# Kernel tuning notes

Measured on AMD Instinct MI355X. Metric: run time of the kernel, lower is better.

## Reference

```python
import jax, jax.numpy as jnp
import numpy as np

B, C, T = 4, 512, 4096
N2 = 32          # d_state // 2 complex modes
H = 2048         # hidden_channels
EPS = 1e-5


def setup_inputs() -> dict:
    key = jax.random.key(0)
    ks = jax.random.split(key, 8)
    dt_min, dt_max = 1e-3, 1e-1
    log_dt = jax.random.uniform(ks[1], (C,)) * (np.log(dt_max) - np.log(dt_min)) + np.log(dt_min)
    return {
        "x": jax.random.normal(ks[0], (B, C, T), jnp.float32),
        # ChannelwiseLayerNorm affine params
        "gamma": jnp.ones((C,), jnp.float32),
        "beta": jnp.zeros((C,), jnp.float32),
        # S4D kernel params (standard S4D-Lin init)
        "log_dt": log_dt.astype(jnp.float32),
        "C_re": jax.random.normal(ks[2], (C, N2), jnp.float32),
        "C_im": jax.random.normal(ks[3], (C, N2), jnp.float32),
        "log_A_real": jnp.log(0.5 * jnp.ones((C, N2), jnp.float32)),
        "A_imag": jnp.tile(jnp.pi * jnp.arange(N2, dtype=jnp.float32), (C, 1)),
        "D": jax.random.normal(ks[4], (C,), jnp.float32),
        # S4D output linear (Conv1d k=1 -> 2C, then GLU over channels)
        "Wo": jax.random.normal(ks[5], (2 * C, C), jnp.float32) / np.sqrt(C),
        "bo": jnp.zeros((2 * C,), jnp.float32),
        # FC MLP: Linear(C->H), PReLU(H), Linear(H->C)
        "W1": jax.random.normal(ks[6], (H, C), jnp.float32) / np.sqrt(C),
        "b1": jnp.zeros((H,), jnp.float32),
        "prelu_a": 0.25 * jnp.ones((H,), jnp.float32),
        "W2": jax.random.normal(ks[7], (C, H), jnp.float32) / np.sqrt(H),
        "b2": jnp.zeros((C,), jnp.float32),
    }


def reference(x, gamma, beta, log_dt, C_re, C_im, log_A_real, A_imag, D,
              Wo, bo, W1, b1, prelu_a, W2, b2):
    # ---- ChannelwiseLayerNorm over the channel dim of [B, C, T] ----
    mean = jnp.mean(x, axis=1, keepdims=True)
    var = jnp.var(x, axis=1, keepdims=True)
    u = gamma[None, :, None] * (x - mean) * jax.lax.rsqrt(var + EPS) + beta[None, :, None]

    # ---- S4D: diagonal SSM kernel via Vandermonde, applied by FFT conv ----
    L = x.shape[-1]
    dt = jnp.exp(log_dt)[:, None]                       # [C, 1]
    A = -jnp.exp(log_A_real) + 1j * A_imag              # [C, N2] complex diag
    dtA = A * dt                                        # [C, N2]
    Cd = (C_re + 1j * C_im) * (jnp.exp(dtA) - 1.0) / A  # discretized C (ZOH)
    vand = jnp.exp(dtA[..., None] * jnp.arange(L, dtype=jnp.float32))  # [C, N2, L]
    K = 2.0 * jnp.einsum('hn,hnl->hl', Cd, vand).real   # [C, L]

    k_f = jnp.fft.rfft(K, n=2 * L)                      # [C, L+1]
    u_f = jnp.fft.rfft(u, n=2 * L)                      # [B, C, L+1]
    y = jnp.fft.irfft(u_f * k_f, n=2 * L)[..., :L]      # causal conv
    y = y + u * D[None, :, None]                        # skip connection
    y = jax.nn.gelu(y, approximate=False)
    # output linear (1x1 conv to 2C) + GLU over channel dim
    z = jnp.einsum('oc,bct->bot', Wo, y) + bo[None, :, None]
    y = z[:, :C] * jax.nn.sigmoid(z[:, C:])             # [B, C, T]

    # ---- FC MLP with PReLU (per hidden channel) ----
    y = y.transpose(0, 2, 1)                            # [B, T, C]
    h = y @ W1.T + b1                                   # [B, T, H]
    h = jnp.where(h >= 0, h, prelu_a * h)
    y = h @ W2.T + b2                                   # [B, T, C]

    return x + y.transpose(0, 2, 1)                     # residual, [B, C, T]
```

## Files before the change

### kernel.cpp

```cpp
#include <hip/hip_runtime.h>
#include <math.h>

#define BB 4
#define CC 512
#define TT 4096
#define NN2 32
#define HH 2048

typedef __bf16 bf8v __attribute__((ext_vector_type(8)));
typedef __bf16 bf4v __attribute__((ext_vector_type(4)));
typedef float  f4v  __attribute__((ext_vector_type(4)));
typedef unsigned short u16x8 __attribute__((ext_vector_type(8)));

__device__ __forceinline__ void gload16(const void* g, void* l){
  __builtin_amdgcn_global_load_lds(
      (const __attribute__((address_space(1))) unsigned int*)g,
      (__attribute__((address_space(3))) unsigned int*)l, 16, 0, 0);
}
__device__ __forceinline__ float fast_gelu(float v){
  float x2 = v*v;
  float x  = 0.7978845608f*v*fmaf(0.044715f, x2, 1.0f);
  float t  = __expf(2.0f*x);
  return v - v*__builtin_amdgcn_rcpf(1.0f + t);
}
__device__ __forceinline__ float fast_sigmoid(float g){
  return __builtin_amdgcn_rcpf(1.0f + __expf(-g));
}
__device__ __forceinline__ unsigned short bfbits(float v){
  __bf16 h = (__bf16)v;
  return __builtin_bit_cast(unsigned short, h);
}

__global__ __launch_bounds__(256) void ln_kernel(
    const float* __restrict__ x, const float* __restrict__ gamma,
    const float* __restrict__ beta, __bf16* __restrict__ u)
{
  int tile = blockIdx.x & 63;
  int b    = blockIdx.x >> 6;
  int tl = threadIdx.x & 15;
  int cg = threadIdx.x >> 4;
  const float4* xp = (const float4*)(x + (size_t)b*CC*TT + tile*64) + tl;
  float4 s = {0,0,0,0}, s2 = {0,0,0,0};
  #pragma unroll 4
  for (int c = cg*32; c < (cg+1)*32; ++c){
    float4 v = xp[(size_t)c*(TT/4)];
    s.x += v.x; s.y += v.y; s.z += v.z; s.w += v.w;
    s2.x = fmaf(v.x,v.x,s2.x); s2.y = fmaf(v.y,v.y,s2.y);
    s2.z = fmaf(v.z,v.z,s2.z); s2.w = fmaf(v.w,v.w,s2.w);
  }
  __shared__ float4 ls[16][16], ls2[16][16], mean_s[16], inv_s[16];
  ls[cg][tl] = s; ls2[cg][tl] = s2;
  __syncthreads();
  if (threadIdx.x < 16){
    float4 ss = {0,0,0,0}, ss2 = {0,0,0,0};
    #pragma unroll
    for (int g2 = 0; g2 < 16; ++g2){
      float4 a = ls[g2][threadIdx.x], b2 = ls2[g2][threadIdx.x];
      ss.x+=a.x; ss.y+=a.y; ss.z+=a.z; ss.w+=a.w;
      ss2.x+=b2.x; ss2.y+=b2.y; ss2.z+=b2.z; ss2.w+=b2.w;
    }
    float4 mn, iv;
    mn.x = ss.x*(1.f/CC); mn.y = ss.y*(1.f/CC); mn.z = ss.z*(1.f/CC); mn.w = ss.w*(1.f/CC);
    iv.x = rsqrtf(ss2.x*(1.f/CC) - mn.x*mn.x + 1e-5f);
    iv.y = rsqrtf(ss2.y*(1.f/CC) - mn.y*mn.y + 1e-5f);
    iv.z = rsqrtf(ss2.z*(1.f/CC) - mn.z*mn.z + 1e-5f);
    iv.w = rsqrtf(ss2.w*(1.f/CC) - mn.w*mn.w + 1e-5f);
    mean_s[threadIdx.x] = mn; inv_s[threadIdx.x] = iv;
  }
  __syncthreads();
  float4 mn = mean_s[tl], iv = inv_s[tl];
  __bf16* up = u + (size_t)b*CC*TT + tile*64 + tl*4;
  #pragma unroll 4
  for (int c = cg*32; c < (cg+1)*32; ++c){
    float4 v = xp[(size_t)c*(TT/4)];
    float gi = gamma[c], be = beta[c];
    bf4v o;
    o[0] = (__bf16)fmaf(gi*iv.x, v.x - mn.x, be);
    o[1] = (__bf16)fmaf(gi*iv.y, v.y - mn.y, be);
    o[2] = (__bf16)fmaf(gi*iv.z, v.z - mn.z, be);
    o[3] = (__bf16)fmaf(gi*iv.w, v.w - mn.w, be);
    *(bf4v*)&up[(size_t)c*TT] = o;
  }
}

__global__ __launch_bounds__(256) void build_mats(
    const float* __restrict__ log_dt, const float* __restrict__ C_re,
    const float* __restrict__ C_im, const float* __restrict__ log_A_real,
    const float* __restrict__ A_imag, const float* __restrict__ Dp,
    __bf16* __restrict__ Tt, __bf16* __restrict__ V, __bf16* __restrict__ B2)
{
  __shared__ float cpart[4][64][33];
  __shared__ float kk[4][65];
  const int wv = threadIdx.x >> 6, lane = threadIdx.x & 63;
  const int c = blockIdx.x*4 + wv;
  const int m = lane & 31;
  float dt = expf(log_dt[c]);
  float Ar = -expf(log_A_real[c*NN2+m]);
  float Ai = A_imag[c*NN2+m];
  float er = expf(Ar*dt);
  float sw_, cw_; sincosf(Ai*dt, &sw_, &cw_);
  float wre = er*cw_, wim = er*sw_;
  float nr = wre-1.f, ni = wim;
  float inv = 1.f/(Ar*Ar + Ai*Ai);
  float qr = (nr*Ar + ni*Ai)*inv;
  float qi = (ni*Ar - nr*Ai)*inv;
  float Cr = C_re[c*NN2+m], Ci = C_im[c*NN2+m];
  float okr =  2.f*(Cr*qr - Ci*qi);
  float oki = -2.f*(Cr*qi + Ci*qr);
  __bf16* Ttc = Tt + (size_t)c*4096;
  __bf16* Vc  = V  + (size_t)c*4096;
  __bf16* B2c = B2 + (size_t)c*4096;
  if (lane < 32){
    float pre = 1.f, pim = 0.f;
    for (int l = 0; l <= 64; ++l){
      if (l <= 63){
        Vc[(2*m)*64   + (63-l)] = (__bf16)pre;
        Vc[(2*m+1)*64 + (63-l)] = (__bf16)pim;
      }
      float cR = fmaf(okr, pre,  oki*pim);
      float cQ = fmaf(oki, pre, -okr*pim);
      if (l <= 63) cpart[wv][l][m] = cR;
      if (l >= 1){
        B2c[(l-1)*64 + 2*m]   = (__bf16)cR;
        B2c[(l-1)*64 + 2*m+1] = (__bf16)cQ;
      }
      float npre = wre*pre - wim*pim;
      float npim = wre*pim + wim*pre;
      pre = npre; pim = npim;
    }
  }
  __syncthreads();
  float s = 0.f;
  #pragma unroll
  for (int mm = 0; mm < 32; ++mm) s += cpart[wv][lane][mm];
  if (lane == 0) s += Dp[c];
  kk[wv][lane] = s;
  __syncthreads();
  const int n = lane;
  #pragma unroll
  for (int kb = 0; kb < 8; ++kb){
    u16x8 v;
    #pragma unroll
    for (int e = 0; e < 8; ++e){
      int k = kb*8 + e;
      v[e] = bfbits((n >= k) ? kk[wv][n-k] : 0.f);
    }
    *(u16x8*)&Ttc[n*64 + kb*8] = v;
  }
}

__global__ __launch_bounds__(128) void s4dm_kernel(
    const __bf16* __restrict__ u, const float* __restrict__ log_dt,
    const float* __restrict__ log_A_real, const float* __restrict__ A_imag,
    const __bf16* __restrict__ Tt, const __bf16* __restrict__ V,
    const __bf16* __restrict__ B2, __bf16* __restrict__ gout)
{
  __shared__ __align__(16) float gbuf[2][64][66];
  __shared__ __align__(16) unsigned short s0buf[2][64][72];
  const int wv = threadIdx.x >> 6, l = threadIdx.x & 63;
  const int lr = l & 15, q = l >> 4;
  const int seq = blockIdx.x*2 + wv;
  const int c = seq & (CC-1);
  const __bf16* Up  = u  + (size_t)seq*TT;
  const __bf16* Ttc = Tt + (size_t)c*4096;
  const __bf16* Vc  = V  + (size_t)c*4096;
  const __bf16* B2c = B2 + (size_t)c*4096;

  f4v acc[4][4];
  #pragma unroll
  for (int a=0;a<4;++a)
    #pragma unroll
    for (int b=0;b<4;++b)
      #pragma unroll
      for (int r=0;r<4;++r) acc[a][b][r] = 0.f;

  #pragma unroll
  for (int kw = 0; kw < 2; ++kw){
    bf8v af[4], bv[4];
    #pragma unroll
    for (int mt=0;mt<4;++mt)
      af[mt] = *(const bf8v*)(Up + (mt*16+lr)*64 + kw*32 + q*8);
    #pragma unroll
    for (int nt=0;nt<4;++nt)
      bv[nt] = *(const bf8v*)(Vc + (nt*16+lr)*64 + kw*32 + q*8);
    #pragma unroll
    for (int mt=0;mt<4;++mt)
      #pragma unroll
      for (int nt=0;nt<4;++nt)
        acc[mt][nt] = __builtin_amdgcn_mfma_f32_16x16x32_bf16(af[mt], bv[nt], acc[mt][nt], 0,0,0);
  }
  #pragma unroll
  for (int mt=0;mt<4;++mt)
    #pragma unroll
    for (int nt=0;nt<4;++nt)
      #pragma unroll
      for (int r=0;r<4;++r)
        gbuf[wv][mt*16 + q*4 + r][nt*16 + lr] = acc[mt][nt][r];
  __syncthreads();

  if (l < 32){
    const int m = l;
    float dt = expf(log_dt[c]);
    float Ar = -expf(log_A_real[c*NN2+m]);
    float Ai = A_imag[c*NN2+m];
    float er = expf(Ar*dt);
    float sw_, cw_; sincosf(Ai*dt, &sw_, &cw_);
    float wr_ = er*cw_, wi_ = er*sw_;
    #pragma unroll
    for (int sq2=0;sq2<6;++sq2){
      float a=wr_, b=wi_;
      wr_ = a*a - b*b; wi_ = 2.f*a*b;
    }
    float S0r=0.f, S0i=0.f;
    for (int j=0;j<64;++j){
      float gr = gbuf[wv][j][2*m], gi = gbuf[wv][j][2*m+1];
      s0buf[wv][j][2*m]   = bfbits(S0r);
      s0buf[wv][j][2*m+1] = bfbits(S0i);
      float nRe = fmaf(wr_, S0r, fmaf(-wi_, S0i, gr));
      float nIm = fmaf(wr_, S0i, fmaf( wi_, S0r, gi));
      S0r = nRe; S0i = nIm;
    }
  }
  __syncthreads();

  #pragma unroll
  for (int a=0;a<4;++a)
    #pragma unroll
    for (int b=0;b<4;++b)
      #pragma unroll
      for (int r=0;r<4;++r) acc[a][b][r] = 0.f;
  #pragma unroll
  for (int kw = 0; kw < 2; ++kw){
    bf8v af[4], bv[4];
    #pragma unroll
    for (int mt=0;mt<4;++mt)
      af[mt] = *(const bf8v*)(Up + (mt*16+lr)*64 + kw*32 + q*8);
    #pragma unroll
    for (int nt=0;nt<4;++nt)
      bv[nt] = *(const bf8v*)(Ttc + (nt*16+lr)*64 + kw*32 + q*8);
    #pragma unroll
    for (int mt=0;mt<4;++mt)
      #pragma unroll
      for (int nt=0;nt<4;++nt)
        acc[mt][nt] = __builtin_amdgcn_mfma_f32_16x16x32_bf16(af[mt], bv[nt], acc[mt][nt], 0,0,0);
  }
  #pragma unroll
  for (int kw = 0; kw < 2; ++kw){
    bf8v af[4], bv[4];
    #pragma unroll
    for (int mt=0;mt<4;++mt)
      af[mt] = *(const bf8v*)&s0buf[wv][mt*16+lr][kw*32 + q*8];
    #pragma unroll
    for (int nt=0;nt<4;++nt)
      bv[nt] = *(const bf8v*)(B2c + (nt*16+lr)*64 + kw*32 + q*8);
    #pragma unroll
    for (int mt=0;mt<4;++mt)
      #pragma unroll
      for (int nt=0;nt<4;++nt)
        acc[mt][nt] = __builtin_amdgcn_mfma_f32_16x16x32_bf16(af[mt], bv[nt], acc[mt][nt], 0,0,0);
  }
  __syncthreads();

  unsigned short (*ybuf)[72] = (unsigned short(*)[72])&gbuf[wv][0][0];
  #pragma unroll
  for (int mt=0;mt<4;++mt)
    #pragma unroll
    for (int nt=0;nt<4;++nt)
      #pragma unroll
      for (int r=0;r<4;++r)
        ybuf[mt*16 + q*4 + r][nt*16 + lr] = bfbits(fast_gelu(acc[mt][nt][r]));
  __syncthreads();
  u16x8* dst = (u16x8*)(gout + (size_t)seq*TT);
  for (int i = l; i < 512; i += 64){
    int row = i >> 3, cq = i & 7;
    dst[i] = *(const u16x8*)&ybuf[row][cq*8];
  }
}

__global__ __launch_bounds__(256) void tr_kernel(const __bf16* __restrict__ gin,
                                                 __bf16* __restrict__ gout)
{
  __shared__ __align__(16) unsigned short ts[64][72];
  int bt = blockIdx.x;
  int bc = blockIdx.y;
  int b  = blockIdx.z;
  int tid = threadIdx.x;
  const __bf16* gp = gin + ((size_t)b*CC + bc*64)*TT + (size_t)bt*64;
  for (int i = tid; i < 512; i += 256){
    int c = i >> 3, tq = i & 7;
    u16x8 v = *(const u16x8*)(gp + (size_t)c*TT + tq*8);
    #pragma unroll
    for (int s = 0; s < 8; ++s) ts[tq*8+s][c] = v[s];
  }
  __syncthreads();
  __bf16* op = gout + ((size_t)b*TT + bt*64)*CC + bc*64;
  for (int i = tid; i < 512; i += 256){
    int t = i >> 3, cq = i & 7;
    u16x8 v = *(const u16x8*)&ts[t][cq*8];
    *(u16x8*)(op + (size_t)t*CC + cq*8) = v;
  }
}

__global__ __launch_bounds__(256) void cvt_kernel(const float4* __restrict__ in,
                                                  bf4v* __restrict__ out, int n4)
{
  int i = blockIdx.x*256 + threadIdx.x;
  if (i < n4){
    float4 v = in[i];
    bf4v o; o[0]=(__bf16)v.x; o[1]=(__bf16)v.y; o[2]=(__bf16)v.z; o[3]=(__bf16)v.w;
    out[i] = o;
  }
}

template<int MODE>
__global__ __launch_bounds__(512, 2) void mm_kernel(
    const __bf16* __restrict__ Aw, const __bf16* __restrict__ Bt,
    const float* __restrict__ bias, const float* __restrict__ aux,
    void* __restrict__ outp)
{
  constexpr int K  = (MODE==2) ? 2048 : 512;
  constexpr int NT = K/32;
  constexpr int LOGGM = (MODE==1) ? 4 : 2;
  constexpr int GM = 1 << LOGGM;
  constexpr int NBUF  = (MODE==0) ? 2 : 3;
  constexpr int DEPTH = NBUF - 1;

  __shared__ __align__(16) __bf16 As[NBUF*128*32];
  __shared__ __align__(16) __bf16 Bs[NBUF*256*32];
  __shared__ __align__(16) __bf16 As2[(MODE==0)?NBUF*128*32:8];

  const int bid = blockIdx.x;
  const int X = bid & 7, L = bid >> 3;
  const int m0 = (L & (GM-1)) * 128;
  const int n0 = (X*8 + (L >> LOGGM)) * 256;

  const int tid = threadIdx.x;
  const int l = tid & 63;
  const int lr = l & 15, kh = l >> 4;
  const int w = tid >> 6;
  const int wm = w >> 2, wn = w & 3;
  const int coff = (kh ^ ((lr ^ (lr >> 2)) & 3)) * 16;

  f4v acc[4][4];
  f4v acc2[(MODE==0)?4:1][(MODE==0)?4:1];
  #pragma unroll
  for (int a=0;a<4;++a)
    #pragma unroll
    for (int b=0;b<4;++b)
      #pragma unroll
      for (int r=0;r<4;++r) acc[a][b][r] = 0.f;
  if constexpr (MODE==0){
    #pragma unroll
    for (int a=0;a<4;++a)
      #pragma unroll
      for (int b=0;b<4;++b)
        #pragma unroll
        for (int r=0;r<4;++r) acc2[a][b][r] = 0.f;
  }

  const char* pA  = (const char*)Aw;
  const char* pA2 = (const char*)(Aw + (size_t)CC*K);
  const char* pB  = (const char*)Bt;

  auto stage = [&](int d, int kt){
    {
      int cch = tid;
      int row = cch >> 2;
      int kb = ((cch & 3) ^ ((row ^ (row >> 2)) & 3)) * 16;
      gload16(pA + ((size_t)(m0+row)*K + kt*32)*2 + kb, (char*)As + d*8192 + cch*16);
      if constexpr (MODE==0)
        gload16(pA2 + ((size_t)(m0+row)*K + kt*32)*2 + kb, (char*)As2 + d*8192 + cch*16);
    }
    #pragma unroll
    for (int i=0;i<2;++i){
      int cch = i*512 + tid;
      int row = cch >> 2;
      int kb = ((cch & 3) ^ ((row ^ (row >> 2)) & 3)) * 16;
      gload16(pB + ((size_t)(n0+row)*K + kt*32)*2 + kb, (char*)Bs + d*16384 + cch*16);
    }
  };

  auto vwait = [&](int ahead){
    if constexpr (MODE==0){
      if (ahead >= 1) asm volatile("s_waitcnt vmcnt(4)" ::: "memory");
      else            asm volatile("s_waitcnt vmcnt(0)" ::: "memory");
    } else {
      if (ahead >= 2)      asm volatile("s_waitcnt vmcnt(6)" ::: "memory");
      else if (ahead == 1) asm volatile("s_waitcnt vmcnt(3)" ::: "memory");
      else                 asm volatile("s_waitcnt vmcnt(0)" ::: "memory");
    }
  };

  auto compute = [&](int d){
    bf8v af[4], bv4[4];
    #pragma unroll
    for (int mi=0;mi<4;++mi){
      int row = wm*64 + mi*16 + lr;
      af[mi] = *(const bf8v*)((const char*)As + d*8192 + row*64 + coff);
    }
    #pragma unroll
    for (int ni=0;ni<4;++ni){
      int row = wn*64 + ni*16 + lr;
      bv4[ni] = *(const bf8v*)((const char*)Bs + d*16384 + row*64 + coff);
    }
    if constexpr (MODE==0){
      bf8v af2[4];
      #pragma unroll
      for (int mi=0;mi<4;++mi){
        int row = wm*64 + mi*16 + lr;
        af2[mi] = *(const bf8v*)((const char*)As2 + d*8192 + row*64 + coff);
      }
      __builtin_amdgcn_s_setprio(1);
      #pragma unroll
      for (int mi=0;mi<4;++mi)
        #pragma unroll
        for (int ni=0;ni<4;++ni){
          acc [mi][ni] = __builtin_amdgcn_mfma_f32_16x16x32_bf16(af [mi], bv4[ni], acc [mi][ni], 0,0,0);
          acc2[mi][ni] = __builtin_amdgcn_mfma_f32_16x16x32_bf16(af2[mi], bv4[ni], acc2[mi][ni], 0,0,0);
        }
      __builtin_amdgcn_s_setprio(0);
    } else {
      __builtin_amdgcn_s_setprio(1);
      #pragma unroll
      for (int mi=0;mi<4;++mi)
        #pragma unroll
        for (int ni=0;ni<4;++ni)
          acc[mi][ni] = __builtin_amdgcn_mfma_f32_16x16x32_bf16(af[mi], bv4[ni], acc[mi][ni], 0,0,0);
      __builtin_amdgcn_s_setprio(0);
    }
  };

  #pragma unroll
  for (int i = 0; i < DEPTH; ++i) stage(i, i);
  #pragma unroll 1
  for (int kt = 0; kt < NT; ++kt){
    if (kt + DEPTH < NT) stage((kt+DEPTH)%NBUF, kt+DEPTH);
    int ahead = NT-1-kt; ahead = (ahead > DEPTH) ? DEPTH : ahead;
    vwait(ahead);
    __builtin_amdgcn_s_barrier();
    compute(kt % NBUF);
    __builtin_amdgcn_s_barrier();
  }

  if constexpr (MODE==0 || MODE==1){
    const int COUT = (MODE==0) ? CC : HH;
    __bf16* O = (__bf16*)outp;
    #pragma unroll
    for (int mi=0;mi<4;++mi){
      int m = m0 + wm*64 + mi*16 + kh*4;
      float4 bi = *(const float4*)&bias[m];
      float bia[4] = {bi.x, bi.y, bi.z, bi.w};
      float gta[4], paa[4];
      if constexpr (MODE==0){
        float4 bg = *(const float4*)&bias[CC + m];
        gta[0]=bg.x; gta[1]=bg.y; gta[2]=bg.z; gta[3]=bg.w;
      } else {
        float4 pa = *(const float4*)&aux[m];
        paa[0]=pa.x; paa[1]=pa.y; paa[2]=pa.z; paa[3]=pa.w;
      }
      #pragma unroll
      for (int ni=0;ni<4;++ni){
        int tok = n0 + wn*64 + ni*16 + lr;
        bf4v o;
        #pragma unroll
        for (int r=0;r<4;++r){
          float v = acc[mi][ni][r] + bia[r];
          if constexpr (MODE==0){
            float gate = acc2[mi][ni][r] + gta[r];
            v = v * fast_sigmoid(gate);
          } else {
            v = (v >= 0.f) ? v : paa[r]*v;
          }
          o[r] = (__bf16)v;
        }
        *(bf4v*)&O[(size_t)tok*COUT + m] = o;
      }
    }
  } else {
    float* O = (float*)outp;
    #pragma unroll
    for (int mi=0;mi<4;++mi){
      int chb = m0 + wm*64 + mi*16 + kh*4;
      float4 bi = *(const float4*)&bias[chb];
      float bia[4] = {bi.x, bi.y, bi.z, bi.w};
      #pragma unroll
      for (int ni=0;ni<4;++ni){
        int tok = n0 + wn*64 + ni*16 + lr;
        int b = tok >> 12, t = tok & 4095;
        size_t rb = ((size_t)(b*CC + chb))*TT + t;
        #pragma unroll
        for (int r=0;r<4;++r)
          O[rb + (size_t)r*TT] = acc[mi][ni][r] + bia[r] + aux[rb + (size_t)r*TT];
      }
    }
  }
}

extern "C" void kernel_launch(void* const* d_in, const int* in_sizes, int n_in,
                              void* d_out, int out_size, void* d_ws, size_t ws_size,
                              hipStream_t stream)
{
  const float* x          = (const float*)d_in[0];
  const float* gamma      = (const float*)d_in[1];
  const float* beta       = (const float*)d_in[2];
  const float* log_dt     = (const float*)d_in[3];
  const float* C_re       = (const float*)d_in[4];
  const float* C_im       = (const float*)d_in[5];
  const float* log_A_real = (const float*)d_in[6];
  const float* A_imag     = (const float*)d_in[7];
  const float* Dp         = (const float*)d_in[8];
  const float* Wo         = (const float*)d_in[9];
  const float* bo         = (const float*)d_in[10];
  const float* W1         = (const float*)d_in[11];
  const float* b1         = (const float*)d_in[12];
  const float* prelu_a    = (const float*)d_in[13];
  const float* W2         = (const float*)d_in[14];
  const float* b2         = (const float*)d_in[15];
  float* out = (float*)d_out;

  char* base = (char*)d_ws;
  const size_t SEGB = (size_t)BB*CC*TT*2;
  __bf16* u_bf  = (__bf16*)(base);
  __bf16* glu   = (__bf16*)(base);
  __bf16* g_cm  = (__bf16*)(base + SEGB);
  __bf16* g_tm  = (__bf16*)(base + 2*SEGB);
  __bf16* h     = (__bf16*)(base + SEGB);
  __bf16* Tt_all = (__bf16*)(base + 2*SEGB);
  __bf16* V_all  = Tt_all + (size_t)CC*4096;
  __bf16* B2_all = V_all  + (size_t)CC*4096;
  __bf16* Wo_bf = (__bf16*)(base + 5*SEGB);
  __bf16* W1_bf = Wo_bf + (size_t)2*CC*CC;
  __bf16* W2_bf = W1_bf + (size_t)HH*CC;

  cvt_kernel<<<dim3((2*CC*CC/4 + 255)/256), 256, 0, stream>>>((const float4*)Wo, (bf4v*)Wo_bf, 2*CC*CC/4);
  cvt_kernel<<<dim3((HH*CC/4 + 255)/256), 256, 0, stream>>>((const float4*)W1, (bf4v*)W1_bf, HH*CC/4);
  cvt_kernel<<<dim3((CC*HH/4 + 255)/256), 256, 0, stream>>>((const float4*)W2, (bf4v*)W2_bf, CC*HH/4);

  build_mats<<<dim3(CC/4), 256, 0, stream>>>(log_dt, C_re, C_im, log_A_real,
                                             A_imag, Dp, Tt_all, V_all, B2_all);
  ln_kernel<<<dim3(BB*(TT/64)), 256, 0, stream>>>(x, gamma, beta, u_bf);
  s4dm_kernel<<<dim3((BB*CC)/2), 128, 0, stream>>>(u_bf, log_dt, log_A_real, A_imag,
                                                   Tt_all, V_all, B2_all, g_cm);
  tr_kernel<<<dim3(TT/64, CC/64, BB), 256, 0, stream>>>(g_cm, g_tm);

  mm_kernel<0><<<dim3(4*64),  512, 0, stream>>>(Wo_bf, g_tm, bo, nullptr, (void*)glu);
  mm_kernel<1><<<dim3(16*64), 512, 0, stream>>>(W1_bf, glu, b1, prelu_a, (void*)h);
  mm_kernel<2><<<dim3(4*64),  512, 0, stream>>>(W2_bf, h, b2, x, (void*)out);
}
```

Measured before the change: 213.7 us.

## Shrink GEMM tiles to 128x128 with 256 threads and double buffering

Reworks the three bf16 MFMA GEMM kernels from 128x256 tiles with 512 threads and 2-3 stage pipelines to 128x128 tiles with 256 threads (2x2 waves) and a fixed two-buffer pipeline, doubling the grid size. The aim is more blocks for better CU occupancy and load balance, and lower LDS use per block. The cost is less reuse per block, since A tiles are reloaded twice as often, and a shallower prefetch depth that may expose more memory latency.

```diff
diff --git a/kernel.cpp b/kernel.cpp
--- a/kernel.cpp
+++ b/kernel.cpp
@@ -313,7 +313,7 @@
 }
 
 template<int MODE>
-__global__ __launch_bounds__(512, 2) void mm_kernel(
+__global__ __launch_bounds__(256) void mm_kernel(
     const __bf16* __restrict__ Aw, const __bf16* __restrict__ Bt,
     const float* __restrict__ bias, const float* __restrict__ aux,
     void* __restrict__ outp)
@@ -322,23 +322,22 @@
   constexpr int NT = K/32;
   constexpr int LOGGM = (MODE==1) ? 4 : 2;
   constexpr int GM = 1 << LOGGM;
-  constexpr int NBUF  = (MODE==0) ? 2 : 3;
-  constexpr int DEPTH = NBUF - 1;
-
-  __shared__ __align__(16) __bf16 As[NBUF*128*32];
-  __shared__ __align__(16) __bf16 Bs[NBUF*256*32];
-  __shared__ __align__(16) __bf16 As2[(MODE==0)?NBUF*128*32:8];
+  constexpr int LPS = (MODE==0) ? 6 : 4;
+
+  __shared__ __align__(16) __bf16 As[2*128*32];
+  __shared__ __align__(16) __bf16 Bs[2*128*32];
+  __shared__ __align__(16) __bf16 As2[(MODE==0)?2*128*32:8];
 
   const int bid = blockIdx.x;
   const int X = bid & 7, L = bid >> 3;
   const int m0 = (L & (GM-1)) * 128;
-  const int n0 = (X*8 + (L >> LOGGM)) * 256;
+  const int n0 = (X*16 + (L >> LOGGM)) * 128;
 
   const int tid = threadIdx.x;
   const int l = tid & 63;
   const int lr = l & 15, kh = l >> 4;
   const int w = tid >> 6;
-  const int wm = w >> 2, wn = w & 3;
+  const int wr = w >> 1, wc = w & 1;
   const int coff = (kh ^ ((lr ^ (lr >> 2)) & 3)) * 16;
 
   f4v acc[4][4];
@@ -363,51 +362,35 @@
   const char* pB  = (const char*)Bt;
 
   auto stage = [&](int d, int kt){
-    {
-      int cch = tid;
+    #pragma unroll
+    for (int i=0;i<2;++i){
+      int cch = i*256 + tid;
       int row = cch >> 2;
       int kb = ((cch & 3) ^ ((row ^ (row >> 2)) & 3)) * 16;
       gload16(pA + ((size_t)(m0+row)*K + kt*32)*2 + kb, (char*)As + d*8192 + cch*16);
+      gload16(pB + ((size_t)(n0+row)*K + kt*32)*2 + kb, (char*)Bs + d*8192 + cch*16);
       if constexpr (MODE==0)
         gload16(pA2 + ((size_t)(m0+row)*K + kt*32)*2 + kb, (char*)As2 + d*8192 + cch*16);
     }
-    #pragma unroll
-    for (int i=0;i<2;++i){
-      int cch = i*512 + tid;
-      int row = cch >> 2;
-      int kb = ((cch & 3) ^ ((row ^ (row >> 2)) & 3)) * 16;
-      gload16(pB + ((size_t)(n0+row)*K + kt*32)*2 + kb, (char*)Bs + d*16384 + cch*16);
-    }
-  };
-
-  auto vwait = [&](int ahead){
-    if constexpr (MODE==0){
-      if (ahead >= 1) asm volatile("s_waitcnt vmcnt(4)" ::: "memory");
-      else            asm volatile("s_waitcnt vmcnt(0)" ::: "memory");
-    } else {
-      if (ahead >= 2)      asm volatile("s_waitcnt vmcnt(6)" ::: "memory");
-      else if (ahead == 1) asm volatile("s_waitcnt vmcnt(3)" ::: "memory");
-      else                 asm volatile("s_waitcnt vmcnt(0)" ::: "memory");
-    }
   };
 
   auto compute = [&](int d){
     bf8v af[4], bv4[4];
     #pragma unroll
     for (int mi=0;mi<4;++mi){
-      int row = wm*64 + mi*16 + lr;
+      int row = wr*64 + mi*16 + lr;
       af[mi] = *(const bf8v*)((const char*)As + d*8192 + row*64 + coff);
     }
     #pragma unroll
     for (int ni=0;ni<4;++ni){
-      int row = wn*64 + ni*16 + lr;
-      bv4[ni] = *(const bf8v*)((const char*)Bs + d*16384 + row*64 + coff);
+      int row = wc*64 + ni*16 + lr;
+      bv4[ni] = *(const bf8v*)((const char*)Bs + d*8192 + row*64 + coff);
     }
     if constexpr (MODE==0){
       bf8v af2[4];
       #pragma unroll
       for (int mi=0;mi<4;++mi){
-        int row = wm*64 + mi*16 + lr;
+        int row = wr*64 + mi*16 + lr;
         af2[mi] = *(const bf8v*)((const char*)As2 + d*8192 + row*64 + coff);
       }
       __builtin_amdgcn_s_setprio(1);
@@ -430,15 +413,17 @@
     }
   };
 
-  #pragma unroll
-  for (int i = 0; i < DEPTH; ++i) stage(i, i);
+  stage(0, 0);
   #pragma unroll 1
   for (int kt = 0; kt < NT; ++kt){
-    if (kt + DEPTH < NT) stage((kt+DEPTH)%NBUF, kt+DEPTH);
-    int ahead = NT-1-kt; ahead = (ahead > DEPTH) ? DEPTH : ahead;
-    vwait(ahead);
+    if (kt + 1 < NT){
+      stage((kt+1)&1, kt+1);
+      asm volatile("s_waitcnt vmcnt(%0)" :: "n"(LPS) : "memory");
+    } else {
+      asm volatile("s_waitcnt vmcnt(0)" ::: "memory");
+    }
     __builtin_amdgcn_s_barrier();
-    compute(kt % NBUF);
+    compute(kt & 1);
     __builtin_amdgcn_s_barrier();
   }
 
@@ -447,7 +432,7 @@
     __bf16* O = (__bf16*)outp;
     #pragma unroll
     for (int mi=0;mi<4;++mi){
-      int m = m0 + wm*64 + mi*16 + kh*4;
+      int m = m0 + wr*64 + mi*16 + kh*4;
       float4 bi = *(const float4*)&bias[m];
       float bia[4] = {bi.x, bi.y, bi.z, bi.w};
       float gta[4], paa[4];
@@ -460,7 +445,7 @@
       }
       #pragma unroll
       for (int ni=0;ni<4;++ni){
-        int tok = n0 + wn*64 + ni*16 + lr;
+        int tok = n0 + wc*64 + ni*16 + lr;
         bf4v o;
         #pragma unroll
         for (int r=0;r<4;++r){
@@ -480,12 +465,12 @@
     float* O = (float*)outp;
     #pragma unroll
     for (int mi=0;mi<4;++mi){
-      int chb = m0 + wm*64 + mi*16 + kh*4;
+      int chb = m0 + wr*64 + mi*16 + kh*4;
       float4 bi = *(const float4*)&bias[chb];
       float bia[4] = {bi.x, bi.y, bi.z, bi.w};
       #pragma unroll
       for (int ni=0;ni<4;++ni){
-        int tok = n0 + wn*64 + ni*16 + lr;
+        int tok = n0 + wc*64 + ni*16 + lr;
         int b = tok >> 12, t = tok & 4095;
         size_t rb = ((size_t)(b*CC + chb))*TT + t;
         #pragma unroll
@@ -543,7 +528,7 @@
                                                    Tt_all, V_all, B2_all, g_cm);
   tr_kernel<<<dim3(TT/64, CC/64, BB), 256, 0, stream>>>(g_cm, g_tm);
 
-  mm_kernel<0><<<dim3(4*64),  512, 0, stream>>>(Wo_bf, g_tm, bo, nullptr, (void*)glu);
-  mm_kernel<1><<<dim3(16*64), 512, 0, stream>>>(W1_bf, glu, b1, prelu_a, (void*)h);
-  mm_kernel<2><<<dim3(4*64),  512, 0, stream>>>(W2_bf, h, b2, x, (void*)out);
-}
+  mm_kernel<0><<<dim3(4*128),  256, 0, stream>>>(Wo_bf, g_tm, bo, nullptr, (void*)glu);
+  mm_kernel<1><<<dim3(16*128), 256, 0, stream>>>(W1_bf, glu, b1, prelu_a, (void*)h);
+  mm_kernel<2><<<dim3(4*128),  256, 0, stream>>>(W2_bf, h, b2, x, (void*)out);
+}
```

Measured after the change: 218.3 us. 2.1% more time.
